# Optimization experiments

Measured on AMD Instinct MI355X. Metric: run time of the kernel, lower is better.

The kernel has to match this reference:

```python
import jax, jax.numpy as jnp
import numpy as np
import math

C = 256
GROUPS = 32
EPS = 1e-5

def setup_inputs() -> dict:
    key = jax.random.key(0)
    ks = jax.random.split(key, 11)
    B, H, W = 8, 64, 64
    s = 1.0 / math.sqrt(C)
    return {
        "x": jax.random.normal(ks[0], (B, C, H, W), dtype=jnp.float32),
        "gamma": jnp.ones((C,), jnp.float32),
        "beta": jnp.zeros((C,), jnp.float32),
        "wq": jax.random.normal(ks[1], (C, C), jnp.float32) * s,
        "bq": jnp.zeros((C,), jnp.float32),
        "wk": jax.random.normal(ks[2], (C, C), jnp.float32) * s,
        "bk": jnp.zeros((C,), jnp.float32),
        "wv": jax.random.normal(ks[3], (C, C), jnp.float32) * s,
        "bv": jnp.zeros((C,), jnp.float32),
        "wp": jax.random.normal(ks[4], (C, C), jnp.float32) * s,
        "bp": jnp.zeros((C,), jnp.float32),
    }

def _group_norm(x, gamma, beta):
    B, Cc, H, W = x.shape
    xg = x.reshape(B, GROUPS, Cc // GROUPS, H, W)
    mu = xg.mean(axis=(2, 3, 4), keepdims=True)
    var = xg.var(axis=(2, 3, 4), keepdims=True)
    xn = ((xg - mu) * jax.lax.rsqrt(var + EPS)).reshape(B, Cc, H, W)
    return xn * gamma[None, :, None, None] + beta[None, :, None, None]

def reference(x, gamma, beta, wq, bq, wk, bk, wv, bv, wp, bp):
    B, Cc, H, W = x.shape
    T = H * W
    h = _group_norm(x, gamma, beta)           # (B,C,H,W)
    hf = h.reshape(B, Cc, T)                  # (B,C,T)
    # 1x1 convs = per-pixel linear maps over channels
    q = jnp.einsum('oc,bct->bto', wq, hf) + bq           # (B,T,C)
    k = jnp.einsum('oc,bct->bot', wk, hf) + bk[:, None]  # (B,C,T)
    v = jnp.einsum('oc,bct->bto', wv, hf) + bv           # (B,T,C)
    scores = jnp.einsum('btc,bcs->bts', q, k) / math.sqrt(Cc)
    attn = jax.nn.softmax(scores, axis=-1)    # (B,T,T)
    z = jnp.einsum('bts,bsc->btc', attn, v)   # (B,T,C)
    zf = z.transpose(0, 2, 1)                 # (B,C,T)
    proj = jnp.einsum('oc,bct->bot', wp, zf) + bp[:, None]
    return x + proj.reshape(B, Cc, H, W)
```

## Files before the change

### kernel.cpp

```cpp
#include <hip/hip_runtime.h>


typedef unsigned short u16;
typedef unsigned char u8;
typedef __attribute__((ext_vector_type(8))) short short8;
typedef __attribute__((ext_vector_type(4))) float f32x4;

#define MFMA16(a, b, c) __builtin_amdgcn_mfma_f32_16x16x32_bf16((a), (b), (c), 0, 0, 0)
#define MFMA16F8(a, b, c) __builtin_amdgcn_mfma_f32_16x16x32_fp8_fp8((a), (b), (c), 0, 0, 0)

#define GLL16(g, l)                                                            \
  __builtin_amdgcn_global_load_lds(                                            \
      (const __attribute__((address_space(1))) void*)(g),                      \
      (__attribute__((address_space(3))) void*)(l), 16, 0, 0)

#define BAR_VM8()  asm volatile("s_waitcnt vmcnt(8)\n\ts_barrier" ::: "memory")
#define BAR_VM4()  asm volatile("s_waitcnt vmcnt(4)\n\ts_barrier" ::: "memory")
#define BAR_LGKM() asm volatile("s_waitcnt lgkmcnt(0)\n\ts_barrier" ::: "memory")

#define CVT_PK_BF16(dst, lo, hi)                                               \
  asm("v_cvt_pk_bf16_f32 %0, %1, %2" : "=v"(dst) : "v"(lo), "v"(hi))

__device__ __forceinline__ u16 f2bf(float f) {
  union { float f; unsigned u; } v; v.f = f;
  unsigned u = v.u;
  return (u16)((u + 0x7FFFu + ((u >> 16) & 1u)) >> 16);
}

__device__ __forceinline__ u8 f2fp8(float f) {
  int p = __builtin_amdgcn_cvt_pk_fp8_f32(f, f, 0, false);
  return (u8)(p & 0xff);
}

__global__ __launch_bounds__(256) void conv_w(const float* __restrict__ s0,
                                              const float* __restrict__ s1,
                                              const float* __restrict__ s2,
                                              const float* __restrict__ s3,
                                              u16* __restrict__ dst) {
  const int m = blockIdx.y;
  const float* s = (m == 0) ? s0 : (m == 1) ? s1 : (m == 2) ? s2 : s3;
  const int i = (blockIdx.x * 256 + threadIdx.x) * 4;
  float4 v = *(const float4*)(s + i);
  u16* d = dst + m * 65536 + i;
  d[0] = f2bf(v.x); d[1] = f2bf(v.y); d[2] = f2bf(v.z); d[3] = f2bf(v.w);
}

__global__ __launch_bounds__(256) void gn_stats(const float* __restrict__ x,
                                                float2* __restrict__ stats) {
  const int bg = blockIdx.x;
  const float* p = x + (long)bg * 32768;
  const int tid = threadIdx.x;
  float s = 0.f, ss = 0.f;
  #pragma unroll 8
  for (int i = 0; i < 32; ++i) {
    float4 v = *(const float4*)(p + tid * 4 + i * 1024);
    s  += v.x + v.y + v.z + v.w;
    ss += v.x * v.x + v.y * v.y + v.z * v.z + v.w * v.w;
  }
  for (int off = 32; off; off >>= 1) {
    s  += __shfl_down(s, off);
    ss += __shfl_down(ss, off);
  }
  __shared__ float2 red[4];
  if ((tid & 63) == 0) red[tid >> 6] = make_float2(s, ss);
  __syncthreads();
  if (tid == 0) {
    float S  = red[0].x + red[1].x + red[2].x + red[3].x;
    float SS = red[0].y + red[1].y + red[2].y + red[3].y;
    float mean = S * (1.f / 32768.f);
    float var  = SS * (1.f / 32768.f) - mean * mean;
    stats[bg] = make_float2(mean, rsqrtf(var + 1e-5f));
  }
}

__global__ __launch_bounds__(256) void gn_apply(const float* __restrict__ x,
                                                const float2* __restrict__ stats,
                                                const float* __restrict__ gamma,
                                                const float* __restrict__ beta,
                                                u16* __restrict__ h_t) {
  __shared__ float tile[64][65];
  const int tid = threadIdx.x;
  const int b = blockIdx.z, c0 = blockIdx.y * 64, t0 = blockIdx.x * 64;
  {
    const int ci = tid >> 2, tj0 = (tid & 3) * 16;
    const int c = c0 + ci;
    float2 st = stats[b * 32 + (c >> 3)];
    float gm = gamma[c] * st.y;
    float bt = beta[c] - st.x * gm;
    const float* xp = x + ((long)(b * 256 + c) * 4096 + t0 + tj0);
    #pragma unroll
    for (int i = 0; i < 4; ++i) {
      float4 v = *(const float4*)(xp + i * 4);
      tile[ci][tj0 + i * 4 + 0] = v.x * gm + bt;
      tile[ci][tj0 + i * 4 + 1] = v.y * gm + bt;
      tile[ci][tj0 + i * 4 + 2] = v.z * gm + bt;
      tile[ci][tj0 + i * 4 + 3] = v.w * gm + bt;
    }
  }
  __syncthreads();
  {
    const int tj = tid >> 2, ci0 = (tid & 3) * 16;
    u16* hp = h_t + ((long)(b * 4096 + t0 + tj) * 256 + c0 + ci0);
    uint4 o0, o1;
    CVT_PK_BF16(o0.x, tile[ci0 +  0][tj], tile[ci0 +  1][tj]);
    CVT_PK_BF16(o0.y, tile[ci0 +  2][tj], tile[ci0 +  3][tj]);
    CVT_PK_BF16(o0.z, tile[ci0 +  4][tj], tile[ci0 +  5][tj]);
    CVT_PK_BF16(o0.w, tile[ci0 +  6][tj], tile[ci0 +  7][tj]);
    CVT_PK_BF16(o1.x, tile[ci0 +  8][tj], tile[ci0 +  9][tj]);
    CVT_PK_BF16(o1.y, tile[ci0 + 10][tj], tile[ci0 + 11][tj]);
    CVT_PK_BF16(o1.z, tile[ci0 + 12][tj], tile[ci0 + 13][tj]);
    CVT_PK_BF16(o1.w, tile[ci0 + 14][tj], tile[ci0 + 15][tj]);
    *(uint4*)hp = o0;
    *(uint4*)(hp + 8) = o1;
  }
}

template <bool ROW_BIAS, bool RESID>
__global__ __launch_bounds__(256, 2) void gemm_bt(
    const u16* __restrict__ A, long strideAz, const u16* __restrict__ B,
    long strideBz, const float* __restrict__ bias, float scale,
    u16* __restrict__ outb, float* __restrict__ outf,
    const float* __restrict__ resid, long strideOz, int N) {
  __shared__ u16 a_lds[128 * 32];
  __shared__ u16 b_lds[128 * 32];
  const int tid = threadIdx.x, w = tid >> 6, l = tid & 63;
  const int l15 = l & 15, l4 = l >> 4;
  const int bz = blockIdx.z;
  A += bz * strideAz;
  B += bz * strideBz;
  const long obase = (long)bz * strideOz;
  const int m0 = blockIdx.y * 128, n0 = blockIdx.x * 128;
  const int wm = (w >> 1) * 64, wn = (w & 1) * 64;

  f32x4 acc[4][4];
  #pragma unroll
  for (int i = 0; i < 4; ++i)
    #pragma unroll
    for (int j = 0; j < 4; ++j) acc[i][j] = (f32x4)0.f;

  for (int kt = 0; kt < 8; ++kt) {
    const int k0 = kt * 32;
    __syncthreads();
    #pragma unroll
    for (int j = 0; j < 2; ++j) {
      const int r0 = (w * 2 + j) * 16;
      const int row = r0 + (l >> 2);
      const int sg = (l & 3) ^ (row & 3);
      GLL16(A + (long)(m0 + row) * 256 + k0 + sg * 8, a_lds + r0 * 32);
      GLL16(B + (long)(n0 + row) * 256 + k0 + sg * 8, b_lds + r0 * 32);
    }
    __syncthreads();
    short8 af[4], bf[4];
    #pragma unroll
    for (int t = 0; t < 4; ++t) {
      const int ra = wm + t * 16 + l15;
      af[t] = *(const short8*)(a_lds + ra * 32 + ((l4 ^ (ra & 3)) * 8));
      const int rb = wn + t * 16 + l15;
      bf[t] = *(const short8*)(b_lds + rb * 32 + ((l4 ^ (rb & 3)) * 8));
    }
    #pragma unroll
    for (int mt = 0; mt < 4; ++mt)
      #pragma unroll
      for (int nt = 0; nt < 4; ++nt) acc[mt][nt] = MFMA16(af[mt], bf[nt], acc[mt][nt]);
  }

  if (!ROW_BIAS) {
    float bv[4];
    #pragma unroll
    for (int nt = 0; nt < 4; ++nt) bv[nt] = bias[n0 + wn + nt * 16 + l15];
    #pragma unroll
    for (int mt = 0; mt < 4; ++mt)
      #pragma unroll
      for (int nt = 0; nt < 4; ++nt)
        #pragma unroll
        for (int r = 0; r < 4; ++r) {
          const int row = m0 + wm + mt * 16 + l4 * 4 + r;
          const int col = n0 + wn + nt * 16 + l15;
          outb[obase + (long)row * N + col] = f2bf((acc[mt][nt][r] + bv[nt]) * scale);
        }
  } else {
    float bm[4][4];
    #pragma unroll
    for (int mt = 0; mt < 4; ++mt)
      #pragma unroll
      for (int r = 0; r < 4; ++r) bm[mt][r] = bias[m0 + wm + mt * 16 + l4 * 4 + r];
    #pragma unroll
    for (int mt = 0; mt < 4; ++mt)
      #pragma unroll
      for (int nt = 0; nt < 4; ++nt)
        #pragma unroll
        for (int r = 0; r < 4; ++r) {
          const int row = m0 + wm + mt * 16 + l4 * 4 + r;
          const int col = n0 + wn + nt * 16 + l15;
          const long idx = obase + (long)row * N + col;
          float v = acc[mt][nt][r] + bm[mt][r];
          if (RESID) outf[idx] = v + resid[idx];
          else       outb[idx] = f2bf(v);
        }
  }
}

__global__ __launch_bounds__(256, 2) void gemm_qk(
    const u16* __restrict__ A, const u16* __restrict__ Bw,
    const float* __restrict__ bq, const float* __restrict__ bk,
    u8* __restrict__ Qs8, u8* __restrict__ Ks8) {
  __shared__ u16 a_lds[128 * 32];
  __shared__ u16 b_lds[128 * 32];
  const int tid = threadIdx.x, w = tid >> 6, l = tid & 63;
  const int l15 = l & 15, l4 = l >> 4;
  const int m0 = blockIdx.y * 128, n0 = blockIdx.x * 128;
  const int wm = (w >> 1) * 64, wn = (w & 1) * 64;

  f32x4 acc[4][4];
  #pragma unroll
  for (int i = 0; i < 4; ++i)
    #pragma unroll
    for (int j = 0; j < 4; ++j) acc[i][j] = (f32x4)0.f;

  for (int kt = 0; kt < 8; ++kt) {
    const int k0 = kt * 32;
    __syncthreads();
    #pragma unroll
    for (int j = 0; j < 2; ++j) {
      const int r0 = (w * 2 + j) * 16;
      const int row = r0 + (l >> 2);
      const int sg = (l & 3) ^ (row & 3);
      GLL16(A + (long)(m0 + row) * 256 + k0 + sg * 8, a_lds + r0 * 32);
      GLL16(Bw + (long)(n0 + row) * 256 + k0 + sg * 8, b_lds + r0 * 32);
    }
    __syncthreads();
    short8 af[4], bf[4];
    #pragma unroll
    for (int t = 0; t < 4; ++t) {
      const int ra = wm + t * 16 + l15;
      af[t] = *(const short8*)(a_lds + ra * 32 + ((l4 ^ (ra & 3)) * 8));
      const int rb = wn + t * 16 + l15;
      bf[t] = *(const short8*)(b_lds + rb * 32 + ((l4 ^ (rb & 3)) * 8));
    }
    #pragma unroll
    for (int mt = 0; mt < 4; ++mt)
      #pragma unroll
      for (int nt = 0; nt < 4; ++nt) acc[mt][nt] = MFMA16(af[mt], bf[nt], acc[mt][nt]);
  }

  const bool isQ = n0 < 256;
  u8* out = isQ ? Qs8 : Ks8;
  const float* bias = isQ ? bq : bk;
  const float osc = isQ ? 0.25f : 0.36067376022224085f;
  const int nc0 = n0 & 255;
  float bv[4];
  #pragma unroll
  for (int nt = 0; nt < 4; ++nt) bv[nt] = bias[nc0 + wn + nt * 16 + l15];
  #pragma unroll
  for (int mt = 0; mt < 4; ++mt)
    #pragma unroll
    for (int nt = 0; nt < 4; ++nt)
      #pragma unroll
      for (int r = 0; r < 4; ++r) {
        const int row = m0 + wm + mt * 16 + l4 * 4 + r;
        const int col = nc0 + wn + nt * 16 + l15;
        out[(long)row * 256 + col] = f2fp8((acc[mt][nt][r] + bv[nt]) * osc);
      }
}

__global__ __launch_bounds__(256, 2) void attn_kernel(
    const u8* __restrict__ Qs8, const u8* __restrict__ Ks8,
    const u16* __restrict__ Vt, u16* __restrict__ Z) {
  __shared__ u8  k_lds8[16384];
  __shared__ u16 v_lds[16384];
  __shared__ u16 p_lds[64 * 72];
  __shared__ float l_red[256];

  const int tid = threadIdx.x, w = tid >> 6, l = tid & 63;
  const int l15 = l & 15, l4 = l >> 4;
  const int bid = blockIdx.x;
  const int batch = bid & 7;
  const int qt = bid >> 3;
  const int ws0 = (w & 1) * 32, wq0 = (w >> 1) * 32, wcolO = (w & 1) * 128;
  const long qrow_base = (long)batch * 4096 + qt * 64;

  const u8*  kbase = Ks8 + (long)batch * 4096 * 256;
  const u16* vbase = Vt + (long)batch * 256 * 4096;

  long qf[2][8];
  {
    const u8* qp = Qs8 + (qrow_base + wq0) * 256;
    #pragma unroll
    for (int qt2 = 0; qt2 < 2; ++qt2)
      #pragma unroll
      for (int ks = 0; ks < 8; ++ks)
        qf[qt2][ks] = *(const long*)(qp + (qt2 * 16 + l15) * 256 + ks * 32 + l4 * 8);
  }

  const int cvv = 8 * w + (l >> 3);
  const int sgv = (l & 7) ^ (cvv & 7);

  f32x4 o_acc[2][8];
  #pragma unroll
  for (int mt = 0; mt < 2; ++mt)
    #pragma unroll
    for (int nt = 0; nt < 8; ++nt) o_acc[mt][nt] = (f32x4)0.f;
  float rs2[2] = {0.f, 0.f};

  #pragma unroll
  for (int j = 0; j < 4; ++j) {
    const int r0 = (j * 4 + w) * 4;
    const int row = r0 + (l >> 4);
    const int g = (l & 15) ^ (row & 15);
    GLL16(kbase + (long)row * 256 + g * 16, k_lds8 + r0 * 256);
  }
  #pragma unroll
  for (int j = 0; j < 8; ++j) {
    const int c0 = (j * 4 + w) * 8;
    GLL16(vbase + (long)(c0 + (l >> 3)) * 4096 + sgv * 8, v_lds + c0 * 64);
  }

  for (int st = 0; st < 64; ++st) {
    const int snn = ((st + 1) & 63) * 64;

    BAR_VM8();

    f32x4 sacc[2][2];
    #pragma unroll
    for (int i = 0; i < 2; ++i)
      #pragma unroll
      for (int j = 0; j < 2; ++j) sacc[i][j] = (f32x4)0.f;
    __builtin_amdgcn_s_setprio(1);
    #pragma unroll
    for (int ks = 0; ks < 8; ++ks) {
      long kf[2];
      #pragma unroll
      for (int st2 = 0; st2 < 2; ++st2) {
        const int row = ws0 + st2 * 16 + l15;
        const int g = (ks * 2 + (l4 >> 1)) ^ l15;
        kf[st2] = *(const long*)(k_lds8 + row * 256 + g * 16 + (l4 & 1) * 8);
      }
      #pragma unroll
      for (int st2 = 0; st2 < 2; ++st2)
        #pragma unroll
        for (int qt2 = 0; qt2 < 2; ++qt2)
          sacc[st2][qt2] = MFMA16F8(kf[st2], qf[qt2][ks], sacc[st2][qt2]);
    }
    __builtin_amdgcn_s_setprio(0);

    #pragma unroll
    for (int st2 = 0; st2 < 2; ++st2)
      #pragma unroll
      for (int qt2 = 0; qt2 < 2; ++qt2) {
        float e0 = __builtin_exp2f(sacc[st2][qt2][0]);
        float e1 = __builtin_exp2f(sacc[st2][qt2][1]);
        float e2 = __builtin_exp2f(sacc[st2][qt2][2]);
        float e3 = __builtin_exp2f(sacc[st2][qt2][3]);
        rs2[qt2] += (e0 + e1) + (e2 + e3);
        unsigned pw0, pw1;
        CVT_PK_BF16(pw0, e0, e1);
        CVT_PK_BF16(pw1, e2, e3);
        *(uint2*)(p_lds + (wq0 + qt2 * 16 + l15) * 72 + ws0 + st2 * 16 + l4 * 4) =
            make_uint2(pw0, pw1);
      }

    BAR_LGKM();

    #pragma unroll
    for (int j = 0; j < 4; ++j) {
      const int r0 = (j * 4 + w) * 4;
      const int row = r0 + (l >> 4);
      const int g = (l & 15) ^ (row & 15);
      GLL16(kbase + (long)(snn + row) * 256 + g * 16, k_lds8 + r0 * 256);
    }

    BAR_VM4();

    __builtin_amdgcn_s_setprio(1);
    #pragma unroll
    for (int ks2 = 0; ks2 < 2; ++ks2) {
      short8 pa[2];
      #pragma unroll
      for (int mt = 0; mt < 2; ++mt)
        pa[mt] = *(const short8*)(p_lds + (wq0 + mt * 16 + l15) * 72 + ks2 * 32 + l4 * 8);
      #pragma unroll
      for (int nt = 0; nt < 8; ++nt) {
        const int c = wcolO + nt * 16 + l15;
        const int gv = (ks2 * 4 + l4) ^ (c & 7);
        short8 vb = *(const short8*)(v_lds + c * 64 + gv * 8);
        #pragma unroll
        for (int mt = 0; mt < 2; ++mt) o_acc[mt][nt] = MFMA16(pa[mt], vb, o_acc[mt][nt]);
      }
    }
    __builtin_amdgcn_s_setprio(0);

    BAR_LGKM();

    #pragma unroll
    for (int j = 0; j < 8; ++j) {
      const int c0 = (j * 4 + w) * 8;
      GLL16(vbase + (long)(c0 + (l >> 3)) * 4096 + snn + sgv * 8, v_lds + c0 * 64);
    }
  }

  #pragma unroll
  for (int qt2 = 0; qt2 < 2; ++qt2) {
    float v = rs2[qt2];
    v += __shfl_xor(v, 16);
    v += __shfl_xor(v, 32);
    if (l4 == 0) l_red[w * 64 + wq0 + qt2 * 16 + l15] = v;
  }
  __syncthreads();
  if (tid < 64) {
    const int w0 = (tid >> 5) * 2;
    float t = l_red[w0 * 64 + tid] + l_red[(w0 + 1) * 64 + tid];
    l_red[tid] = 1.f / t;
  }
  __syncthreads();

  #pragma unroll
  for (int mt = 0; mt < 2; ++mt) {
    float inv[4];
    #pragma unroll
    for (int r = 0; r < 4; ++r) inv[r] = l_red[wq0 + mt * 16 + l4 * 4 + r];
    #pragma unroll
    for (int nt = 0; nt < 8; ++nt) {
      const int col = wcolO + nt * 16 + l15;
      #pragma unroll
      for (int r = 0; r < 4; ++r) {
        const long row = qrow_base + wq0 + mt * 16 + l4 * 4 + r;
        Z[row * 256 + col] = f2bf(o_acc[mt][nt][r] * inv[r]);
      }
    }
  }
}

extern "C" void kernel_launch(void* const* d_in, const int* in_sizes, int n_in,
                              void* d_out, int out_size, void* d_ws, size_t ws_size,
                              hipStream_t stream) {
  (void)in_sizes; (void)n_in; (void)out_size; (void)ws_size;
  const float* x     = (const float*)d_in[0];
  const float* gamma = (const float*)d_in[1];
  const float* beta  = (const float*)d_in[2];
  const float* wq    = (const float*)d_in[3];
  const float* bq    = (const float*)d_in[4];
  const float* wk    = (const float*)d_in[5];
  const float* bk    = (const float*)d_in[6];
  const float* wv    = (const float*)d_in[7];
  const float* bv    = (const float*)d_in[8];
  const float* wp    = (const float*)d_in[9];
  const float* bp    = (const float*)d_in[10];
  float* out = (float*)d_out;

  char* ws = (char*)d_ws;
  u16*    wb    = (u16*)(ws);
  float2* stats = (float2*)(ws + 524288);
  u16*    h_t   = (u16*)(ws + 526336);
  u8*     Qs8   = (u8*)(ws + 17303552);
  u8*     Ks8   = (u8*)(ws + 25692160);
  u16*    Vt    = (u16*)(ws + 34080768);
  u16*    Zb    = (u16*)(ws + 50857984);

  conv_w<<<dim3(64, 4), dim3(256), 0, stream>>>(wq, wk, wv, wp, wb);
  gn_stats<<<dim3(256), dim3(256), 0, stream>>>(x, stats);
  gn_apply<<<dim3(64, 4, 8), dim3(256), 0, stream>>>(x, stats, gamma, beta, h_t);

  const long sB = 4096L * 256L, sO = 256L * 4096L;
  gemm_qk<<<dim3(4, 256), dim3(256), 0, stream>>>(h_t, wb, bq, bk, Qs8, Ks8);
  gemm_bt<true, false><<<dim3(32, 2, 8), dim3(256), 0, stream>>>(
      wb + 2 * 65536, 0L, h_t, sB, bv, 1.0f, Vt, nullptr, nullptr, sO, 4096);

  attn_kernel<<<dim3(512), dim3(256), 0, stream>>>(Qs8, Ks8, Vt, Zb);

  gemm_bt<true, true><<<dim3(32, 2, 8), dim3(256), 0, stream>>>(
      wb + 3 * 65536, 0L, Zb, sB, bp, 1.0f, nullptr, out, x, sO, 4096);
}
```

Baseline: 290.5 us.

## Double-buffer K/V tiles and use 512-thread blocks covering 128 query rows

Reworks the attention kernel to use 8 waves per block, each block handling 128 query rows, so every K/V tile loaded into LDS is shared by twice as many queries. K and V tiles are now double-buffered, with the next tile's loads issued right after a full vmcnt(0) barrier, replacing the earlier split K/V prefetch with partial waits. This is meant to halve K/V global traffic per query and overlap loads with compute. In exchange it uses more LDS (about 105 KB) and one block per CU, which reduces latency hiding across blocks. The grid shrinks to 256 blocks.

After: 312.6 us. 7.6% more time.

```diff
diff --git a/kernel.cpp b/kernel.cpp
--- a/kernel.cpp
+++ b/kernel.cpp
@@ -14,8 +14,7 @@
       (const __attribute__((address_space(1))) void*)(g),                      \
       (__attribute__((address_space(3))) void*)(l), 16, 0, 0)
 
-#define BAR_VM8()  asm volatile("s_waitcnt vmcnt(8)\n\ts_barrier" ::: "memory")
-#define BAR_VM4()  asm volatile("s_waitcnt vmcnt(4)\n\ts_barrier" ::: "memory")
+#define BAR_VM0()  asm volatile("s_waitcnt vmcnt(0)\n\ts_barrier" ::: "memory")
 #define BAR_LGKM() asm volatile("s_waitcnt lgkmcnt(0)\n\ts_barrier" ::: "memory")
 
 #define CVT_PK_BF16(dst, lo, hi)                                               \
@@ -263,13 +262,13 @@
       }
 }
 
-__global__ __launch_bounds__(256, 2) void attn_kernel(
+__global__ __launch_bounds__(512, 1) void attn_kernel(
     const u8* __restrict__ Qs8, const u8* __restrict__ Ks8,
     const u16* __restrict__ Vt, u16* __restrict__ Z) {
-  __shared__ u8  k_lds8[16384];
-  __shared__ u16 v_lds[16384];
-  __shared__ u16 p_lds[64 * 72];
-  __shared__ float l_red[256];
+  __shared__ u8  k_lds8[2][16384];
+  __shared__ u16 v_lds[2][16384];
+  __shared__ u16 p_lds[128 * 72];
+  __shared__ float l_red[384];
 
   const int tid = threadIdx.x, w = tid >> 6, l = tid & 63;
   const int l15 = l & 15, l4 = l >> 4;
@@ -277,7 +276,7 @@
   const int batch = bid & 7;
   const int qt = bid >> 3;
   const int ws0 = (w & 1) * 32, wq0 = (w >> 1) * 32, wcolO = (w & 1) * 128;
-  const long qrow_base = (long)batch * 4096 + qt * 64;
+  const long qrow_base = (long)batch * 4096 + qt * 128;
 
   const u8*  kbase = Ks8 + (long)batch * 4096 * 256;
   const u16* vbase = Vt + (long)batch * 256 * 4096;
@@ -292,8 +291,7 @@
         qf[qt2][ks] = *(const long*)(qp + (qt2 * 16 + l15) * 256 + ks * 32 + l4 * 8);
   }
 
-  const int cvv = 8 * w + (l >> 3);
-  const int sgv = (l & 7) ^ (cvv & 7);
+  const int sgv = (l & 7) ^ ((l >> 3) & 7);
 
   f32x4 o_acc[2][8];
   #pragma unroll
@@ -303,22 +301,37 @@
   float rs2[2] = {0.f, 0.f};
 
   #pragma unroll
-  for (int j = 0; j < 4; ++j) {
-    const int r0 = (j * 4 + w) * 4;
+  for (int j = 0; j < 2; ++j) {
+    const int r0 = (j * 8 + w) * 4;
     const int row = r0 + (l >> 4);
     const int g = (l & 15) ^ (row & 15);
-    GLL16(kbase + (long)row * 256 + g * 16, k_lds8 + r0 * 256);
-  }
-  #pragma unroll
-  for (int j = 0; j < 8; ++j) {
-    const int c0 = (j * 4 + w) * 8;
-    GLL16(vbase + (long)(c0 + (l >> 3)) * 4096 + sgv * 8, v_lds + c0 * 64);
+    GLL16(kbase + (long)row * 256 + g * 16, k_lds8[0] + r0 * 256);
+  }
+  #pragma unroll
+  for (int j = 0; j < 4; ++j) {
+    const int c0 = (j * 8 + w) * 8;
+    GLL16(vbase + (long)(c0 + (l >> 3)) * 4096 + sgv * 8, v_lds[0] + c0 * 64);
   }
 
   for (int st = 0; st < 64; ++st) {
+    const int buf = st & 1;
     const int snn = ((st + 1) & 63) * 64;
 
-    BAR_VM8();
+    BAR_VM0();
+
+    #pragma unroll
+    for (int j = 0; j < 2; ++j) {
+      const int r0 = (j * 8 + w) * 4;
+      const int row = r0 + (l >> 4);
+      const int g = (l & 15) ^ (row & 15);
+      GLL16(kbase + (long)(snn + row) * 256 + g * 16, k_lds8[buf ^ 1] + r0 * 256);
+    }
+    #pragma unroll
+    for (int j = 0; j < 4; ++j) {
+      const int c0 = (j * 8 + w) * 8;
+      GLL16(vbase + (long)(c0 + (l >> 3)) * 4096 + snn + sgv * 8,
+            v_lds[buf ^ 1] + c0 * 64);
+    }
 
     f32x4 sacc[2][2];
     #pragma unroll
@@ -333,7 +346,7 @@
       for (int st2 = 0; st2 < 2; ++st2) {
         const int row = ws0 + st2 * 16 + l15;
         const int g = (ks * 2 + (l4 >> 1)) ^ l15;
-        kf[st2] = *(const long*)(k_lds8 + row * 256 + g * 16 + (l4 & 1) * 8);
+        kf[st2] = *(const long*)(k_lds8[buf] + row * 256 + g * 16 + (l4 & 1) * 8);
       }
       #pragma unroll
       for (int st2 = 0; st2 < 2; ++st2)
@@ -361,16 +374,6 @@
 
     BAR_LGKM();
 
-    #pragma unroll
-    for (int j = 0; j < 4; ++j) {
-      const int r0 = (j * 4 + w) * 4;
-      const int row = r0 + (l >> 4);
-      const int g = (l & 15) ^ (row & 15);
-      GLL16(kbase + (long)(snn + row) * 256 + g * 16, k_lds8 + r0 * 256);
-    }
-
-    BAR_VM4();
-
     __builtin_amdgcn_s_setprio(1);
     #pragma unroll
     for (int ks2 = 0; ks2 < 2; ++ks2) {
@@ -382,20 +385,12 @@
       for (int nt = 0; nt < 8; ++nt) {
         const int c = wcolO + nt * 16 + l15;
         const int gv = (ks2 * 4 + l4) ^ (c & 7);
-        short8 vb = *(const short8*)(v_lds + c * 64 + gv * 8);
+        short8 vb = *(const short8*)(v_lds[buf] + c * 64 + gv * 8);
         #pragma unroll
         for (int mt = 0; mt < 2; ++mt) o_acc[mt][nt] = MFMA16(pa[mt], vb, o_acc[mt][nt]);
       }
     }
     __builtin_amdgcn_s_setprio(0);
-
-    BAR_LGKM();
-
-    #pragma unroll
-    for (int j = 0; j < 8; ++j) {
-      const int c0 = (j * 4 + w) * 8;
-      GLL16(vbase + (long)(c0 + (l >> 3)) * 4096 + snn + sgv * 8, v_lds + c0 * 64);
-    }
   }
 
   #pragma unroll
@@ -403,13 +398,13 @@
     float v = rs2[qt2];
     v += __shfl_xor(v, 16);
     v += __shfl_xor(v, 32);
-    if (l4 == 0) l_red[w * 64 + wq0 + qt2 * 16 + l15] = v;
+    if (l4 == 0) l_red[w * 32 + qt2 * 16 + l15] = v;
   }
   __syncthreads();
-  if (tid < 64) {
-    const int w0 = (tid >> 5) * 2;
-    float t = l_red[w0 * 64 + tid] + l_red[(w0 + 1) * 64 + tid];
-    l_red[tid] = 1.f / t;
+  if (tid < 128) {
+    const int m = tid >> 5, qi = tid & 31;
+    float t = l_red[m * 64 + qi] + l_red[m * 64 + 32 + qi];
+    l_red[256 + tid] = 1.f / t;
   }
   __syncthreads();
 
@@ -417,7 +412,7 @@
   for (int mt = 0; mt < 2; ++mt) {
     float inv[4];
     #pragma unroll
-    for (int r = 0; r < 4; ++r) inv[r] = l_red[wq0 + mt * 16 + l4 * 4 + r];
+    for (int r = 0; r < 4; ++r) inv[r] = l_red[256 + wq0 + mt * 16 + l4 * 4 + r];
     #pragma unroll
     for (int nt = 0; nt < 8; ++nt) {
       const int col = wcolO + nt * 16 + l15;
@@ -465,7 +460,7 @@
   gemm_bt<true, false><<<dim3(32, 2, 8), dim3(256), 0, stream>>>(
       wb + 2 * 65536, 0L, h_t, sB, bv, 1.0f, Vt, nullptr, nullptr, sO, 4096);
 
-  attn_kernel<<<dim3(512), dim3(256), 0, stream>>>(Qs8, Ks8, Vt, Zb);
+  attn_kernel<<<dim3(256), dim3(512), 0, stream>>>(Qs8, Ks8, Vt, Zb);
 
   gemm_bt<true, true><<<dim3(32, 2, 8), dim3(256), 0, stream>>>(
       wb + 3 * 65536, 0L, Zb, sB, bp, 1.0f, nullptr, out, x, sO, 4096);
```

## Double-buffer K/V tiles in attention with smaller 32-key steps

Applied to the files above, without the earlier changes.

The attention loop now uses two LDS buffers for K and V and processes 32 keys per iteration instead of 64, doubling the iteration count. Loads for the next tile are issued at the start of each iteration into the other buffer, so the per-phase partial vmcnt waits and the extra barrier become a single full wait per step. This aims to overlap global loads with compute more cleanly. In exchange it adds twice as many barriers overall and halves the MFMA work per synchronisation.

After: 319.6 us. +10.0%, slower.

```diff
diff --git a/kernel.cpp b/kernel.cpp
--- a/kernel.cpp
+++ b/kernel.cpp
@@ -14,8 +14,7 @@
       (const __attribute__((address_space(1))) void*)(g),                      \
       (__attribute__((address_space(3))) void*)(l), 16, 0, 0)
 
-#define BAR_VM8()  asm volatile("s_waitcnt vmcnt(8)\n\ts_barrier" ::: "memory")
-#define BAR_VM4()  asm volatile("s_waitcnt vmcnt(4)\n\ts_barrier" ::: "memory")
+#define BAR_VM0()  asm volatile("s_waitcnt vmcnt(0)\n\ts_barrier" ::: "memory")
 #define BAR_LGKM() asm volatile("s_waitcnt lgkmcnt(0)\n\ts_barrier" ::: "memory")
 
 #define CVT_PK_BF16(dst, lo, hi)                                               \
@@ -266,9 +265,9 @@
 __global__ __launch_bounds__(256, 2) void attn_kernel(
     const u8* __restrict__ Qs8, const u8* __restrict__ Ks8,
     const u16* __restrict__ Vt, u16* __restrict__ Z) {
-  __shared__ u8  k_lds8[16384];
-  __shared__ u16 v_lds[16384];
-  __shared__ u16 p_lds[64 * 72];
+  __shared__ u8  k_lds8[2][8192];
+  __shared__ u16 v_lds[2][8192];
+  __shared__ u16 p_lds[64 * 40];
   __shared__ float l_red[256];
 
   const int tid = threadIdx.x, w = tid >> 6, l = tid & 63;
@@ -276,7 +275,7 @@
   const int bid = blockIdx.x;
   const int batch = bid & 7;
   const int qt = bid >> 3;
-  const int ws0 = (w & 1) * 32, wq0 = (w >> 1) * 32, wcolO = (w & 1) * 128;
+  const int ws0 = (w & 1) * 16, wq0 = (w >> 1) * 32, wcolO = (w & 1) * 128;
   const long qrow_base = (long)batch * 4096 + qt * 64;
 
   const u8*  kbase = Ks8 + (long)batch * 4096 * 256;
@@ -292,8 +291,9 @@
         qf[qt2][ks] = *(const long*)(qp + (qt2 * 16 + l15) * 256 + ks * 32 + l4 * 8);
   }
 
-  const int cvv = 8 * w + (l >> 3);
-  const int sgv = (l & 7) ^ (cvv & 7);
+  const int krow_in = l >> 4;
+  const int vrow_in = l >> 2;
+  const int vgs = (l & 3) ^ ((l >> 2) & 3);
 
   f32x4 o_acc[2][8];
   #pragma unroll
@@ -303,99 +303,81 @@
   float rs2[2] = {0.f, 0.f};
 
   #pragma unroll
+  for (int j = 0; j < 2; ++j) {
+    const int r0 = (j * 4 + w) * 4;
+    const int row = r0 + krow_in;
+    const int g = (l & 15) ^ (row & 15);
+    GLL16(kbase + (long)row * 256 + g * 16, k_lds8[0] + r0 * 256);
+  }
+  #pragma unroll
   for (int j = 0; j < 4; ++j) {
-    const int r0 = (j * 4 + w) * 4;
-    const int row = r0 + (l >> 4);
-    const int g = (l & 15) ^ (row & 15);
-    GLL16(kbase + (long)row * 256 + g * 16, k_lds8 + r0 * 256);
-  }
-  #pragma unroll
-  for (int j = 0; j < 8; ++j) {
-    const int c0 = (j * 4 + w) * 8;
-    GLL16(vbase + (long)(c0 + (l >> 3)) * 4096 + sgv * 8, v_lds + c0 * 64);
-  }
-
-  for (int st = 0; st < 64; ++st) {
-    const int snn = ((st + 1) & 63) * 64;
-
-    BAR_VM8();
-
-    f32x4 sacc[2][2];
-    #pragma unroll
-    for (int i = 0; i < 2; ++i)
-      #pragma unroll
-      for (int j = 0; j < 2; ++j) sacc[i][j] = (f32x4)0.f;
+    const int idx = j * 4 + w;
+    const int cv = idx * 16 + vrow_in;
+    GLL16(vbase + (long)cv * 4096 + vgs * 8, v_lds[0] + idx * 512);
+  }
+
+  for (int st = 0; st < 128; ++st) {
+    const int buf = st & 1;
+    const int sn = ((st + 1) & 127) * 32;
+
+    BAR_VM0();
+
+    #pragma unroll
+    for (int j = 0; j < 2; ++j) {
+      const int r0 = (j * 4 + w) * 4;
+      const int row = r0 + krow_in;
+      const int g = (l & 15) ^ (row & 15);
+      GLL16(kbase + (long)(sn + row) * 256 + g * 16, k_lds8[buf ^ 1] + r0 * 256);
+    }
+    #pragma unroll
+    for (int j = 0; j < 4; ++j) {
+      const int idx = j * 4 + w;
+      const int cv = idx * 16 + vrow_in;
+      GLL16(vbase + (long)cv * 4096 + sn + vgs * 8, v_lds[buf ^ 1] + idx * 512);
+    }
+
+    f32x4 sacc[2];
+    sacc[0] = (f32x4)0.f;
+    sacc[1] = (f32x4)0.f;
     __builtin_amdgcn_s_setprio(1);
     #pragma unroll
     for (int ks = 0; ks < 8; ++ks) {
-      long kf[2];
-      #pragma unroll
-      for (int st2 = 0; st2 < 2; ++st2) {
-        const int row = ws0 + st2 * 16 + l15;
-        const int g = (ks * 2 + (l4 >> 1)) ^ l15;
-        kf[st2] = *(const long*)(k_lds8 + row * 256 + g * 16 + (l4 & 1) * 8);
-      }
-      #pragma unroll
-      for (int st2 = 0; st2 < 2; ++st2)
-        #pragma unroll
-        for (int qt2 = 0; qt2 < 2; ++qt2)
-          sacc[st2][qt2] = MFMA16F8(kf[st2], qf[qt2][ks], sacc[st2][qt2]);
+      const int g = (ks * 2 + (l4 >> 1)) ^ l15;
+      long kf = *(const long*)(k_lds8[buf] + (ws0 + l15) * 256 + g * 16 + (l4 & 1) * 8);
+      sacc[0] = MFMA16F8(kf, qf[0][ks], sacc[0]);
+      sacc[1] = MFMA16F8(kf, qf[1][ks], sacc[1]);
     }
     __builtin_amdgcn_s_setprio(0);
 
     #pragma unroll
-    for (int st2 = 0; st2 < 2; ++st2)
-      #pragma unroll
-      for (int qt2 = 0; qt2 < 2; ++qt2) {
-        float e0 = __builtin_exp2f(sacc[st2][qt2][0]);
-        float e1 = __builtin_exp2f(sacc[st2][qt2][1]);
-        float e2 = __builtin_exp2f(sacc[st2][qt2][2]);
-        float e3 = __builtin_exp2f(sacc[st2][qt2][3]);
-        rs2[qt2] += (e0 + e1) + (e2 + e3);
-        unsigned pw0, pw1;
-        CVT_PK_BF16(pw0, e0, e1);
-        CVT_PK_BF16(pw1, e2, e3);
-        *(uint2*)(p_lds + (wq0 + qt2 * 16 + l15) * 72 + ws0 + st2 * 16 + l4 * 4) =
-            make_uint2(pw0, pw1);
-      }
+    for (int qt2 = 0; qt2 < 2; ++qt2) {
+      float e0 = __builtin_exp2f(sacc[qt2][0]);
+      float e1 = __builtin_exp2f(sacc[qt2][1]);
+      float e2 = __builtin_exp2f(sacc[qt2][2]);
+      float e3 = __builtin_exp2f(sacc[qt2][3]);
+      rs2[qt2] += (e0 + e1) + (e2 + e3);
+      unsigned pw0, pw1;
+      CVT_PK_BF16(pw0, e0, e1);
+      CVT_PK_BF16(pw1, e2, e3);
+      *(uint2*)(p_lds + (wq0 + qt2 * 16 + l15) * 40 + ws0 + l4 * 4) =
+          make_uint2(pw0, pw1);
+    }
 
     BAR_LGKM();
 
-    #pragma unroll
-    for (int j = 0; j < 4; ++j) {
-      const int r0 = (j * 4 + w) * 4;
-      const int row = r0 + (l >> 4);
-      const int g = (l & 15) ^ (row & 15);
-      GLL16(kbase + (long)(snn + row) * 256 + g * 16, k_lds8 + r0 * 256);
-    }
-
-    BAR_VM4();
-
     __builtin_amdgcn_s_setprio(1);
-    #pragma unroll
-    for (int ks2 = 0; ks2 < 2; ++ks2) {
-      short8 pa[2];
-      #pragma unroll
-      for (int mt = 0; mt < 2; ++mt)
-        pa[mt] = *(const short8*)(p_lds + (wq0 + mt * 16 + l15) * 72 + ks2 * 32 + l4 * 8);
-      #pragma unroll
-      for (int nt = 0; nt < 8; ++nt) {
-        const int c = wcolO + nt * 16 + l15;
-        const int gv = (ks2 * 4 + l4) ^ (c & 7);
-        short8 vb = *(const short8*)(v_lds + c * 64 + gv * 8);
-        #pragma unroll
-        for (int mt = 0; mt < 2; ++mt) o_acc[mt][nt] = MFMA16(pa[mt], vb, o_acc[mt][nt]);
-      }
+    short8 pa[2];
+    #pragma unroll
+    for (int mt = 0; mt < 2; ++mt)
+      pa[mt] = *(const short8*)(p_lds + (wq0 + mt * 16 + l15) * 40 + l4 * 8);
+    #pragma unroll
+    for (int nt = 0; nt < 8; ++nt) {
+      const int c = wcolO + nt * 16 + l15;
+      short8 vb = *(const short8*)(v_lds[buf] + c * 32 + ((l4 ^ (c & 3)) * 8));
+      #pragma unroll
+      for (int mt = 0; mt < 2; ++mt) o_acc[mt][nt] = MFMA16(pa[mt], vb, o_acc[mt][nt]);
     }
     __builtin_amdgcn_s_setprio(0);
-
-    BAR_LGKM();
-
-    #pragma unroll
-    for (int j = 0; j < 8; ++j) {
-      const int c0 = (j * 4 + w) * 8;
-      GLL16(vbase + (long)(c0 + (l >> 3)) * 4096 + snn + sgv * 8, v_lds + c0 * 64);
-    }
   }
 
   #pragma unroll
```

## Give each wave its own 16 query rows and pass P through registers

Applied to the files above, without the earlier changes.

Repartitions the attention kernel so each wave owns 16 query rows across all 64 keys and all 256 output channels, instead of a 2x2 split over queries and keys. The softmax numerators now stay in registers and are rearranged into the MFMA A-operand layout with ds_bpermute, which removes the P round-trip through LDS and the cross-wave row-sum reduction. V is double-buffered in LDS so the next tile's load overlaps the current PV step, and the waits become a full vmcnt(0) barrier plus a bare barrier. In exchange each wave reads all of V from LDS for every tile (more LDS traffic), keeps 16 output accumulators live (more registers), and uses extra LDS for the second V buffer, which may reduce occupancy.

New measurement: 333.2 us. 1.15x slower.

```diff
diff --git a/kernel.cpp b/kernel.cpp
--- a/kernel.cpp
+++ b/kernel.cpp
@@ -5,6 +5,7 @@
 typedef unsigned char u8;
 typedef __attribute__((ext_vector_type(8))) short short8;
 typedef __attribute__((ext_vector_type(4))) float f32x4;
+typedef __attribute__((ext_vector_type(4))) int i32x4;
 
 #define MFMA16(a, b, c) __builtin_amdgcn_mfma_f32_16x16x32_bf16((a), (b), (c), 0, 0, 0)
 #define MFMA16F8(a, b, c) __builtin_amdgcn_mfma_f32_16x16x32_fp8_fp8((a), (b), (c), 0, 0, 0)
@@ -14,9 +15,8 @@
       (const __attribute__((address_space(1))) void*)(g),                      \
       (__attribute__((address_space(3))) void*)(l), 16, 0, 0)
 
-#define BAR_VM8()  asm volatile("s_waitcnt vmcnt(8)\n\ts_barrier" ::: "memory")
-#define BAR_VM4()  asm volatile("s_waitcnt vmcnt(4)\n\ts_barrier" ::: "memory")
-#define BAR_LGKM() asm volatile("s_waitcnt lgkmcnt(0)\n\ts_barrier" ::: "memory")
+#define BAR_VM0()  asm volatile("s_waitcnt vmcnt(0)\n\ts_barrier" ::: "memory")
+#define BAR_BARE() asm volatile("s_barrier" ::: "memory")
 
 #define CVT_PK_BF16(dst, lo, hi)                                               \
   asm("v_cvt_pk_bf16_f32 %0, %1, %2" : "=v"(dst) : "v"(lo), "v"(hi))
@@ -267,41 +267,41 @@
     const u8* __restrict__ Qs8, const u8* __restrict__ Ks8,
     const u16* __restrict__ Vt, u16* __restrict__ Z) {
   __shared__ u8  k_lds8[16384];
-  __shared__ u16 v_lds[16384];
-  __shared__ u16 p_lds[64 * 72];
-  __shared__ float l_red[256];
+  __shared__ u16 v_lds[2][16384];
 
   const int tid = threadIdx.x, w = tid >> 6, l = tid & 63;
   const int l15 = l & 15, l4 = l >> 4;
   const int bid = blockIdx.x;
   const int batch = bid & 7;
   const int qt = bid >> 3;
-  const int ws0 = (w & 1) * 32, wq0 = (w >> 1) * 32, wcolO = (w & 1) * 128;
+  const int wq0 = w * 16;
   const long qrow_base = (long)batch * 4096 + qt * 64;
 
   const u8*  kbase = Ks8 + (long)batch * 4096 * 256;
   const u16* vbase = Vt + (long)batch * 256 * 4096;
 
-  long qf[2][8];
+  long qf[8];
   {
-    const u8* qp = Qs8 + (qrow_base + wq0) * 256;
-    #pragma unroll
-    for (int qt2 = 0; qt2 < 2; ++qt2)
-      #pragma unroll
-      for (int ks = 0; ks < 8; ++ks)
-        qf[qt2][ks] = *(const long*)(qp + (qt2 * 16 + l15) * 256 + ks * 32 + l4 * 8);
-  }
-
-  const int cvv = 8 * w + (l >> 3);
-  const int sgv = (l & 7) ^ (cvv & 7);
-
-  f32x4 o_acc[2][8];
-  #pragma unroll
-  for (int mt = 0; mt < 2; ++mt)
-    #pragma unroll
-    for (int nt = 0; nt < 8; ++nt) o_acc[mt][nt] = (f32x4)0.f;
-  float rs2[2] = {0.f, 0.f};
-
+    const u8* qp = Qs8 + (qrow_base + wq0 + l15) * 256 + l4 * 8;
+    #pragma unroll
+    for (int ks = 0; ks < 8; ++ks) qf[ks] = *(const long*)(qp + ks * 32);
+  }
+
+  const int sgv = (l & 7) ^ ((l >> 3) & 7);
+  const int idx0 = (((2 * l4) & 3) * 16 + l15) << 2;
+  const int idx1 = (((2 * l4 + 1) & 3) * 16 + l15) << 2;
+  const bool hi = (l4 >= 2);
+
+  f32x4 o_acc[16];
+  #pragma unroll
+  for (int nt = 0; nt < 16; ++nt) o_acc[nt] = (f32x4)0.f;
+  float rs = 0.f;
+
+  #pragma unroll
+  for (int j = 0; j < 8; ++j) {
+    const int c0 = (j * 4 + w) * 8;
+    GLL16(vbase + (long)(c0 + (l >> 3)) * 4096 + sgv * 8, v_lds[0] + c0 * 64);
+  }
   #pragma unroll
   for (int j = 0; j < 4; ++j) {
     const int r0 = (j * 4 + w) * 4;
@@ -309,123 +309,99 @@
     const int g = (l & 15) ^ (row & 15);
     GLL16(kbase + (long)row * 256 + g * 16, k_lds8 + r0 * 256);
   }
-  #pragma unroll
-  for (int j = 0; j < 8; ++j) {
-    const int c0 = (j * 4 + w) * 8;
-    GLL16(vbase + (long)(c0 + (l >> 3)) * 4096 + sgv * 8, v_lds + c0 * 64);
-  }
 
   for (int st = 0; st < 64; ++st) {
-    const int snn = ((st + 1) & 63) * 64;
-
-    BAR_VM8();
-
-    f32x4 sacc[2][2];
-    #pragma unroll
-    for (int i = 0; i < 2; ++i)
-      #pragma unroll
-      for (int j = 0; j < 2; ++j) sacc[i][j] = (f32x4)0.f;
+    const int buf = st & 1;
+    const int sn = ((st + 1) & 63) * 64;
+
+    BAR_VM0();
+
+    #pragma unroll
+    for (int j = 0; j < 8; ++j) {
+      const int c0 = (j * 4 + w) * 8;
+      GLL16(vbase + (long)(c0 + (l >> 3)) * 4096 + sn + sgv * 8,
+            v_lds[buf ^ 1] + c0 * 64);
+    }
+
+    f32x4 sacc[4];
+    #pragma unroll
+    for (int i = 0; i < 4; ++i) sacc[i] = (f32x4)0.f;
     __builtin_amdgcn_s_setprio(1);
     #pragma unroll
     for (int ks = 0; ks < 8; ++ks) {
-      long kf[2];
-      #pragma unroll
-      for (int st2 = 0; st2 < 2; ++st2) {
-        const int row = ws0 + st2 * 16 + l15;
-        const int g = (ks * 2 + (l4 >> 1)) ^ l15;
-        kf[st2] = *(const long*)(k_lds8 + row * 256 + g * 16 + (l4 & 1) * 8);
+      const int g = (ks * 2 + (l4 >> 1)) ^ l15;
+      #pragma unroll
+      for (int st2 = 0; st2 < 4; ++st2) {
+        long kf = *(const long*)(k_lds8 + (st2 * 16 + l15) * 256 + g * 16 + (l4 & 1) * 8);
+        sacc[st2] = MFMA16F8(kf, qf[ks], sacc[st2]);
       }
-      #pragma unroll
-      for (int st2 = 0; st2 < 2; ++st2)
-        #pragma unroll
-        for (int qt2 = 0; qt2 < 2; ++qt2)
-          sacc[st2][qt2] = MFMA16F8(kf[st2], qf[qt2][ks], sacc[st2][qt2]);
     }
     __builtin_amdgcn_s_setprio(0);
 
-    #pragma unroll
-    for (int st2 = 0; st2 < 2; ++st2)
-      #pragma unroll
-      for (int qt2 = 0; qt2 < 2; ++qt2) {
-        float e0 = __builtin_exp2f(sacc[st2][qt2][0]);
-        float e1 = __builtin_exp2f(sacc[st2][qt2][1]);
-        float e2 = __builtin_exp2f(sacc[st2][qt2][2]);
-        float e3 = __builtin_exp2f(sacc[st2][qt2][3]);
-        rs2[qt2] += (e0 + e1) + (e2 + e3);
-        unsigned pw0, pw1;
-        CVT_PK_BF16(pw0, e0, e1);
-        CVT_PK_BF16(pw1, e2, e3);
-        *(uint2*)(p_lds + (wq0 + qt2 * 16 + l15) * 72 + ws0 + st2 * 16 + l4 * 4) =
-            make_uint2(pw0, pw1);
-      }
-
-    BAR_LGKM();
+    BAR_BARE();
 
     #pragma unroll
     for (int j = 0; j < 4; ++j) {
       const int r0 = (j * 4 + w) * 4;
       const int row = r0 + (l >> 4);
       const int g = (l & 15) ^ (row & 15);
-      GLL16(kbase + (long)(snn + row) * 256 + g * 16, k_lds8 + r0 * 256);
-    }
-
-    BAR_VM4();
+      GLL16(kbase + (long)(sn + row) * 256 + g * 16, k_lds8 + r0 * 256);
+    }
+
+    unsigned wpk[4][2];
+    #pragma unroll
+    for (int st2 = 0; st2 < 4; ++st2) {
+      float e0 = __builtin_exp2f(sacc[st2][0]);
+      float e1 = __builtin_exp2f(sacc[st2][1]);
+      float e2 = __builtin_exp2f(sacc[st2][2]);
+      float e3 = __builtin_exp2f(sacc[st2][3]);
+      rs += (e0 + e1) + (e2 + e3);
+      CVT_PK_BF16(wpk[st2][0], e0, e1);
+      CVT_PK_BF16(wpk[st2][1], e2, e3);
+    }
+
+    short8 pa[2];
+    #pragma unroll
+    for (int ks2 = 0; ks2 < 2; ++ks2) {
+      i32x4 pv;
+      #pragma unroll
+      for (int t = 0; t < 4; ++t) {
+        const int idx = (t < 2) ? idx0 : idx1;
+        int lo = __builtin_amdgcn_ds_bpermute(idx, (int)wpk[2 * ks2][t & 1]);
+        int hv = __builtin_amdgcn_ds_bpermute(idx, (int)wpk[2 * ks2 + 1][t & 1]);
+        pv[t] = hi ? hv : lo;
+      }
+      pa[ks2] = __builtin_bit_cast(short8, pv);
+    }
 
     __builtin_amdgcn_s_setprio(1);
     #pragma unroll
-    for (int ks2 = 0; ks2 < 2; ++ks2) {
-      short8 pa[2];
-      #pragma unroll
-      for (int mt = 0; mt < 2; ++mt)
-        pa[mt] = *(const short8*)(p_lds + (wq0 + mt * 16 + l15) * 72 + ks2 * 32 + l4 * 8);
-      #pragma unroll
-      for (int nt = 0; nt < 8; ++nt) {
-        const int c = wcolO + nt * 16 + l15;
+    for (int nt = 0; nt < 16; ++nt) {
+      const int c = nt * 16 + l15;
+      #pragma unroll
+      for (int ks2 = 0; ks2 < 2; ++ks2) {
         const int gv = (ks2 * 4 + l4) ^ (c & 7);
-        short8 vb = *(const short8*)(v_lds + c * 64 + gv * 8);
-        #pragma unroll
-        for (int mt = 0; mt < 2; ++mt) o_acc[mt][nt] = MFMA16(pa[mt], vb, o_acc[mt][nt]);
+        short8 vb = *(const short8*)(v_lds[buf] + c * 64 + gv * 8);
+        o_acc[nt] = MFMA16(pa[ks2], vb, o_acc[nt]);
       }
     }
     __builtin_amdgcn_s_setprio(0);
-
-    BAR_LGKM();
-
-    #pragma unroll
-    for (int j = 0; j < 8; ++j) {
-      const int c0 = (j * 4 + w) * 8;
-      GLL16(vbase + (long)(c0 + (l >> 3)) * 4096 + snn + sgv * 8, v_lds + c0 * 64);
-    }
-  }
-
-  #pragma unroll
-  for (int qt2 = 0; qt2 < 2; ++qt2) {
-    float v = rs2[qt2];
-    v += __shfl_xor(v, 16);
-    v += __shfl_xor(v, 32);
-    if (l4 == 0) l_red[w * 64 + wq0 + qt2 * 16 + l15] = v;
-  }
-  __syncthreads();
-  if (tid < 64) {
-    const int w0 = (tid >> 5) * 2;
-    float t = l_red[w0 * 64 + tid] + l_red[(w0 + 1) * 64 + tid];
-    l_red[tid] = 1.f / t;
-  }
-  __syncthreads();
-
-  #pragma unroll
-  for (int mt = 0; mt < 2; ++mt) {
-    float inv[4];
-    #pragma unroll
-    for (int r = 0; r < 4; ++r) inv[r] = l_red[wq0 + mt * 16 + l4 * 4 + r];
-    #pragma unroll
-    for (int nt = 0; nt < 8; ++nt) {
-      const int col = wcolO + nt * 16 + l15;
-      #pragma unroll
-      for (int r = 0; r < 4; ++r) {
-        const long row = qrow_base + wq0 + mt * 16 + l4 * 4 + r;
-        Z[row * 256 + col] = f2bf(o_acc[mt][nt][r] * inv[r]);
-      }
+  }
+
+  float tot = rs;
+  tot += __shfl_xor(tot, 16);
+  tot += __shfl_xor(tot, 32);
+  float inv[4];
+  #pragma unroll
+  for (int r = 0; r < 4; ++r) inv[r] = 1.f / __shfl(tot, l4 * 4 + r);
+
+  #pragma unroll
+  for (int nt = 0; nt < 16; ++nt) {
+    const int col = nt * 16 + l15;
+    #pragma unroll
+    for (int r = 0; r < 4; ++r) {
+      const long row = qrow_base + wq0 + l4 * 4 + r;
+      Z[row * 256 + col] = f2bf(o_acc[nt][r] * inv[r]);
     }
   }
 }
```
